# Optimization experiments

Hardware: AMD Instinct MI355X
Metric: run time of the kernel (lower is better)

Reference implementation:

```python
import jax, jax.numpy as jnp
import numpy as np

EPS = 1e-8  # torchmetrics pairwise_cosine_similarity zero_diagonal-free eps behavior

def _l2_normalize(x, eps=EPS):
    # normalize rows; clamp norm to eps like torchmetrics does
    n = jnp.linalg.norm(x, axis=-1, keepdims=True)
    return x / jnp.maximum(n, eps)

def setup_inputs() -> dict:
    key = jax.random.key(0)
    k1, k2 = jax.random.split(key)
    hvs = jax.random.normal(k1, (16384, 4096), dtype=jnp.float32)  # [N, D] query hypervectors
    am = jax.random.normal(k2, (1024, 4096), dtype=jnp.float32)    # [C, D] associative memory
    return {"hvs": hvs, "am": am}

def reference(hvs, am):
    # pairwise cosine similarity: [N, C]
    sims = jnp.einsum('nd,cd->nc', _l2_normalize(hvs), _l2_normalize(am.astype(jnp.float32)))
    # predict(): top-1 retrieval over classes
    preds = jnp.argmax(sims, axis=1)
    # compute_confidence(): eta = (sims[:,1] - sims[:,0]) / 4 + 1/2
    eta = (sims[:, 1] - sims[:, 0]) * 0.25 + 0.5
    return preds, eta
```

## Files before the change

kernel.cpp:

```cpp
#include <hip/hip_runtime.h>
#include <hip/hip_bf16.h>


#define NQ 16384
#define NC 1024
#define DK 4096
#define TAU 4e-4f
#define WLMAX 8192

typedef __attribute__((ext_vector_type(8))) short short8;
typedef __attribute__((ext_vector_type(4))) float f32x4;
typedef unsigned short ushort_t;

__device__ __forceinline__ unsigned short bf16_rne(float x) {
    unsigned int u = __float_as_uint(x);
    u += 0x7FFFu + ((u >> 16) & 1u);
    return (unsigned short)(u >> 16);
}
__device__ __forceinline__ float bf16_f32(unsigned short h) {
    return __uint_as_float(((unsigned int)h) << 16);
}

#define GLDS(g, l)                                                                       \
    __builtin_amdgcn_global_load_lds((const __attribute__((address_space(1))) void*)(g), \
                                     (__attribute__((address_space(3))) void*)(l), 16, 0, 0)

__global__ void __launch_bounds__(256) norm_all_kernel(const float* __restrict__ hvs,
                                                       const float* __restrict__ am,
                                                       ushort_t* __restrict__ Ah,
                                                       ushort_t* __restrict__ Bh,
                                                       ushort_t* __restrict__ Bl) {
    const int b = blockIdx.x;
    const int tid = threadIdx.x;
    const float* x;
    ushort_t *hp, *lp;
    bool wlo;
    if (b < NC) {
        x = am + (size_t)b * DK;
        hp = Bh + (size_t)b * DK;
        lp = Bl + (size_t)b * DK;
        wlo = true;
    } else {
        const int r = b - NC;
        x = hvs + (size_t)r * DK;
        hp = Ah + (size_t)r * DK;
        lp = nullptr;
        wlo = false;
    }
    const float4* x4 = (const float4*)x;

    float4 v[4];
    float ss = 0.f;
#pragma unroll
    for (int i = 0; i < 4; ++i) {
        v[i] = x4[tid * 4 + i];
        ss += v[i].x * v[i].x + v[i].y * v[i].y + v[i].z * v[i].z + v[i].w * v[i].w;
    }
#pragma unroll
    for (int off = 32; off; off >>= 1) ss += __shfl_xor(ss, off, 64);
    __shared__ float wsum[4];
    const int lane = tid & 63, w = tid >> 6;
    if (lane == 0) wsum[w] = ss;
    __syncthreads();
    const float tot = wsum[0] + wsum[1] + wsum[2] + wsum[3];
    const float r = 1.0f / fmaxf(sqrtf(tot), 1e-8f);

    ushort_t hbuf[16], lbuf[16];
#pragma unroll
    for (int i = 0; i < 4; ++i) {
        const float xs[4] = {v[i].x * r, v[i].y * r, v[i].z * r, v[i].w * r};
#pragma unroll
        for (int j = 0; j < 4; ++j) {
            const unsigned short h = bf16_rne(xs[j]);
            hbuf[i * 4 + j] = h;
            lbuf[i * 4 + j] = bf16_rne(xs[j] - bf16_f32(h));
        }
    }
    ushort_t* hq = hp + tid * 16;
    *(short8*)hq = *(short8*)hbuf;
    *(short8*)(hq + 8) = *(short8*)(hbuf + 8);
    if (wlo) {
        ushort_t* lq = lp + tid * 16;
        *(short8*)lq = *(short8*)lbuf;
        *(short8*)(lq + 8) = *(short8*)(lbuf + 8);
    }
}

__global__ void __launch_bounds__(256, 3) gemm1_kernel(const ushort_t* __restrict__ Ah,
                                                       const ushort_t* __restrict__ Bh,
                                                       float4* __restrict__ cand,
                                                       float* __restrict__ s01) {
    __shared__ __align__(16) ushort_t lA[2][128 * 32];
    __shared__ __align__(16) ushort_t lB[2][128 * 32];

    const int tid = threadIdx.x;
    const int lane = tid & 63;
    const int w = tid >> 6;
    const int wm = w >> 1;
    const int wn = w & 1;

    const int id = blockIdx.x;
    const int xcd = id & 7;
    const int slot = id >> 3;
    const int by = xcd * 16 + (slot >> 3);
    const int bx = slot & 7;

    int sq[2];
    size_t offA[2], offB[2];
#pragma unroll
    for (int i = 0; i < 2; ++i) {
        const int q = tid + i * 256;
        sq[i] = q;
        const int row = q >> 2;
        const int gs = (q & 3) ^ ((row >> 1) & 3);
        offA[i] = (size_t)(by * 128 + row) * DK + gs * 8;
        offB[i] = (size_t)(bx * 128 + row) * DK + gs * 8;
    }

    f32x4 acc[4][4];
#pragma unroll
    for (int m = 0; m < 4; ++m)
#pragma unroll
        for (int n = 0; n < 4; ++n) acc[m][n] = (f32x4){0.f, 0.f, 0.f, 0.f};

    const int r0 = lane & 15;
    const int rg = lane >> 4;

    int aoff[4], boff[4];
#pragma unroll
    for (int m = 0; m < 4; ++m) {
        const int row = wm * 64 + m * 16 + r0;
        aoff[m] = row * 32 + (rg ^ ((row >> 1) & 3)) * 8;
    }
#pragma unroll
    for (int n = 0; n < 4; ++n) {
        const int col = wn * 64 + n * 16 + r0;
        boff[n] = col * 32 + (rg ^ ((col >> 1) & 3)) * 8;
    }

    auto stage = [&](int buf, int kt) {
        const size_t ko = (size_t)kt * 32;
        GLDS(Ah + offA[0] + ko, &lA[buf][sq[0] * 8]);
        GLDS(Ah + offA[1] + ko, &lA[buf][sq[1] * 8]);
        GLDS(Bh + offB[0] + ko, &lB[buf][sq[0] * 8]);
        GLDS(Bh + offB[1] + ko, &lB[buf][sq[1] * 8]);
    };

    stage(0, 0);
    const int nK = DK / 32;
    for (int kt = 0; kt < nK; ++kt) {
        const int cur = kt & 1;
        if (kt + 1 < nK) {
            stage(cur ^ 1, kt + 1);
            asm volatile("s_waitcnt vmcnt(4)" ::: "memory");
        } else {
            asm volatile("s_waitcnt vmcnt(0)" ::: "memory");
        }
        __builtin_amdgcn_s_barrier();

        short8 b0 = *(const short8*)&lB[cur][boff[0]];
        short8 b1 = *(const short8*)&lB[cur][boff[1]];
        short8 b2 = *(const short8*)&lB[cur][boff[2]];
        short8 b3 = *(const short8*)&lB[cur][boff[3]];
        short8 a0 = *(const short8*)&lA[cur][aoff[0]];
        short8 a1 = *(const short8*)&lA[cur][aoff[1]];
        short8 a2 = *(const short8*)&lA[cur][aoff[2]];
        short8 a3 = *(const short8*)&lA[cur][aoff[3]];
        asm volatile("s_waitcnt lgkmcnt(0)" ::: "memory");
        __builtin_amdgcn_s_setprio(1);
        acc[0][0] = __builtin_amdgcn_mfma_f32_16x16x32_bf16(a0, b0, acc[0][0], 0, 0, 0);
        acc[0][1] = __builtin_amdgcn_mfma_f32_16x16x32_bf16(a0, b1, acc[0][1], 0, 0, 0);
        acc[0][2] = __builtin_amdgcn_mfma_f32_16x16x32_bf16(a0, b2, acc[0][2], 0, 0, 0);
        acc[0][3] = __builtin_amdgcn_mfma_f32_16x16x32_bf16(a0, b3, acc[0][3], 0, 0, 0);
        acc[1][0] = __builtin_amdgcn_mfma_f32_16x16x32_bf16(a1, b0, acc[1][0], 0, 0, 0);
        acc[1][1] = __builtin_amdgcn_mfma_f32_16x16x32_bf16(a1, b1, acc[1][1], 0, 0, 0);
        acc[1][2] = __builtin_amdgcn_mfma_f32_16x16x32_bf16(a1, b2, acc[1][2], 0, 0, 0);
        acc[1][3] = __builtin_amdgcn_mfma_f32_16x16x32_bf16(a1, b3, acc[1][3], 0, 0, 0);
        acc[2][0] = __builtin_amdgcn_mfma_f32_16x16x32_bf16(a2, b0, acc[2][0], 0, 0, 0);
        acc[2][1] = __builtin_amdgcn_mfma_f32_16x16x32_bf16(a2, b1, acc[2][1], 0, 0, 0);
        acc[2][2] = __builtin_amdgcn_mfma_f32_16x16x32_bf16(a2, b2, acc[2][2], 0, 0, 0);
        acc[2][3] = __builtin_amdgcn_mfma_f32_16x16x32_bf16(a2, b3, acc[2][3], 0, 0, 0);
        acc[3][0] = __builtin_amdgcn_mfma_f32_16x16x32_bf16(a3, b0, acc[3][0], 0, 0, 0);
        acc[3][1] = __builtin_amdgcn_mfma_f32_16x16x32_bf16(a3, b1, acc[3][1], 0, 0, 0);
        acc[3][2] = __builtin_amdgcn_mfma_f32_16x16x32_bf16(a3, b2, acc[3][2], 0, 0, 0);
        acc[3][3] = __builtin_amdgcn_mfma_f32_16x16x32_bf16(a3, b3, acc[3][3], 0, 0, 0);
        __builtin_amdgcn_s_setprio(0);
        __builtin_amdgcn_s_barrier();
    }

    const int rowb = by * 128 + wm * 64;
#pragma unroll
    for (int m = 0; m < 4; ++m) {
#pragma unroll
        for (int j = 0; j < 4; ++j) {
            float v1 = acc[m][0][j];
            int i1 = bx * 128 + wn * 64 + r0;
            float v2 = -3.402823466e+38f;
#pragma unroll
            for (int n = 1; n < 4; ++n) {
                const float v = acc[m][n][j];
                const int c = bx * 128 + wn * 64 + n * 16 + r0;
                if (v > v1) { v2 = v1; v1 = v; i1 = c; }
                else { v2 = fmaxf(v2, v); }
            }
#pragma unroll
            for (int off = 1; off < 16; off <<= 1) {
                const float o1 = __shfl_xor(v1, off, 64);
                const int oi = __shfl_xor(i1, off, 64);
                const float o2 = __shfl_xor(v2, off, 64);
                if (o1 > v1 || (o1 == v1 && oi < i1)) { v2 = fmaxf(v1, o2); v1 = o1; i1 = oi; }
                else { v2 = fmaxf(v2, o1); }
            }
            const int row = rowb + m * 16 + rg * 4 + j;
            if (r0 == 0)
                cand[(size_t)row * 16 + bx * 2 + wn] = make_float4(v1, (float)i1, v2, 0.f);
            if (bx == 0 && wn == 0 && r0 < 2) s01[row * 2 + r0] = acc[m][0][j];
        }
    }
}

__global__ void __launch_bounds__(256) finalizeA_kernel(const float4* __restrict__ cand,
                                                        const float* __restrict__ s01,
                                                        float* __restrict__ out,
                                                        int* __restrict__ wl,
                                                        int* __restrict__ wc) {
    const int row = blockIdx.x * 256 + threadIdx.x;
    const float4* c = cand + (size_t)row * 16;
    float4 c0 = c[0];
    float M = c0.x, iM = c0.y, M2 = c0.z;
#pragma unroll
    for (int k = 1; k < 16; ++k) {
        const float4 ck = c[k];
        if (ck.x > M) { M2 = fmaxf(M, ck.z); M = ck.x; iM = ck.y; }
        else { M2 = fmaxf(M2, ck.x); }
    }
    out[row] = iM;
    out[NQ + row] = (s01[row * 2 + 1] - s01[row * 2 + 0]) * 0.25f + 0.5f;
    if (M - M2 < TAU) {
        const int p = atomicAdd(wc, 1);
        if (p < WLMAX) wl[p] = row;
    }
}

__global__ void __launch_bounds__(256) recheck_prep_kernel(const float* __restrict__ hvs,
                                                           const int* __restrict__ wl,
                                                           const int* __restrict__ wc,
                                                           ushort_t* __restrict__ A2h,
                                                           ushort_t* __restrict__ A2l) {
    const int cnt = min(*wc, WLMAX);
    const int s = blockIdx.x;
    if (s >= cnt) return;
    const int row = wl[s];
    const int tid = threadIdx.x;
    const float4* x4 = (const float4*)(hvs + (size_t)row * DK);

    float4 v[4];
    float ss = 0.f;
#pragma unroll
    for (int i = 0; i < 4; ++i) {
        v[i] = x4[tid * 4 + i];
        ss += v[i].x * v[i].x + v[i].y * v[i].y + v[i].z * v[i].z + v[i].w * v[i].w;
    }
#pragma unroll
    for (int off = 32; off; off >>= 1) ss += __shfl_xor(ss, off, 64);
    __shared__ float wsum[4];
    const int lane = tid & 63, w = tid >> 6;
    if (lane == 0) wsum[w] = ss;
    __syncthreads();
    const float tot = wsum[0] + wsum[1] + wsum[2] + wsum[3];
    const float r = 1.0f / fmaxf(sqrtf(tot), 1e-8f);

    ushort_t hbuf[16], lbuf[16];
#pragma unroll
    for (int i = 0; i < 4; ++i) {
        const float xs[4] = {v[i].x * r, v[i].y * r, v[i].z * r, v[i].w * r};
#pragma unroll
        for (int j = 0; j < 4; ++j) {
            const unsigned short h = bf16_rne(xs[j]);
            hbuf[i * 4 + j] = h;
            lbuf[i * 4 + j] = bf16_rne(xs[j] - bf16_f32(h));
        }
    }
    ushort_t* hp = A2h + (size_t)s * DK + tid * 16;
    ushort_t* lp = A2l + (size_t)s * DK + tid * 16;
    *(short8*)hp = *(short8*)hbuf;
    *(short8*)(hp + 8) = *(short8*)(hbuf + 8);
    *(short8*)lp = *(short8*)lbuf;
    *(short8*)(lp + 8) = *(short8*)(lbuf + 8);
}

__global__ void __launch_bounds__(512, 2) gemm2_kernel(const ushort_t* __restrict__ A2h,
                                                       const ushort_t* __restrict__ A2l,
                                                       const ushort_t* __restrict__ Bh,
                                                       const ushort_t* __restrict__ Bl,
                                                       const int* __restrict__ wc,
                                                       float2* __restrict__ cand2) {
    const int cnt = min(*wc, WLMAX);
    const int by = blockIdx.y;
    const int bx = blockIdx.x;
    if (by * 128 >= cnt) return;

    __shared__ __align__(16) ushort_t lA[4][2][128 * 32];
    __shared__ __align__(16) ushort_t lB[4][2][128 * 32];

    const int tid = threadIdx.x;
    const int lane = tid & 63;
    const int w = tid >> 6;
    const int wm = w >> 2;
    const int wn = w & 3;
    const int r0 = lane & 15;
    const int rg = lane >> 4;

    const int srow = tid >> 2;
    const int gs = (tid & 3) ^ ((srow >> 1) & 3);
    const size_t offA = (size_t)(by * 128 + srow) * DK + gs * 8;
    const size_t offB = (size_t)(bx * 128 + srow) * DK + gs * 8;

    f32x4 acc[4][2];
#pragma unroll
    for (int m = 0; m < 4; ++m)
#pragma unroll
        for (int n = 0; n < 2; ++n) acc[m][n] = (f32x4){0.f, 0.f, 0.f, 0.f};

    int aoff[4], boff[2];
#pragma unroll
    for (int m = 0; m < 4; ++m) {
        const int row = wm * 64 + m * 16 + r0;
        aoff[m] = row * 32 + (rg ^ ((row >> 1) & 3)) * 8;
    }
#pragma unroll
    for (int n = 0; n < 2; ++n) {
        const int col = wn * 32 + n * 16 + r0;
        boff[n] = col * 32 + (rg ^ ((col >> 1) & 3)) * 8;
    }

    auto stage = [&](int kt) {
        const int buf = kt & 3;
        const size_t ko = (size_t)kt * 32;
        GLDS(A2h + offA + ko, &lA[buf][0][tid * 8]);
        GLDS(A2l + offA + ko, &lA[buf][1][tid * 8]);
        GLDS(Bh + offB + ko, &lB[buf][0][tid * 8]);
        GLDS(Bl + offB + ko, &lB[buf][1][tid * 8]);
    };

    stage(0); stage(1); stage(2);
    const int nK = DK / 32;
    for (int kt = 0; kt < nK; ++kt) {
        const int buf = kt & 3;
        if (kt + 3 < nK) {
            stage(kt + 3);
            asm volatile("s_waitcnt vmcnt(12)" ::: "memory");
        } else if (kt + 3 == nK) {
            asm volatile("s_waitcnt vmcnt(8)" ::: "memory");
        } else if (kt + 2 == nK) {
            asm volatile("s_waitcnt vmcnt(4)" ::: "memory");
        } else {
            asm volatile("s_waitcnt vmcnt(0)" ::: "memory");
        }
        __builtin_amdgcn_s_barrier();

        short8 bh[2], bl[2];
#pragma unroll
        for (int n = 0; n < 2; ++n) {
            bh[n] = *(const short8*)&lB[buf][0][boff[n]];
            bl[n] = *(const short8*)&lB[buf][1][boff[n]];
        }
#pragma unroll
        for (int m = 0; m < 4; ++m) {
            const short8 ah = *(const short8*)&lA[buf][0][aoff[m]];
            const short8 al = *(const short8*)&lA[buf][1][aoff[m]];
#pragma unroll
            for (int n = 0; n < 2; ++n) {
                acc[m][n] = __builtin_amdgcn_mfma_f32_16x16x32_bf16(ah, bh[n], acc[m][n], 0, 0, 0);
                acc[m][n] = __builtin_amdgcn_mfma_f32_16x16x32_bf16(ah, bl[n], acc[m][n], 0, 0, 0);
                acc[m][n] = __builtin_amdgcn_mfma_f32_16x16x32_bf16(al, bh[n], acc[m][n], 0, 0, 0);
            }
        }
        __builtin_amdgcn_s_barrier();
    }

#pragma unroll
    for (int m = 0; m < 4; ++m) {
#pragma unroll
        for (int j = 0; j < 4; ++j) {
            float best = acc[m][0][j];
            int bidx = bx * 128 + wn * 32 + r0;
            {
                const float v = acc[m][1][j];
                const int c = bx * 128 + wn * 32 + 16 + r0;
                if (v > best) { best = v; bidx = c; }
            }
#pragma unroll
            for (int off = 1; off < 16; off <<= 1) {
                const float ov = __shfl_xor(best, off, 64);
                const int oi = __shfl_xor(bidx, off, 64);
                if (ov > best || (ov == best && oi < bidx)) { best = ov; bidx = oi; }
            }
            const int slotg = by * 128 + wm * 64 + m * 16 + rg * 4 + j;
            if (r0 == 0 && slotg < cnt)
                cand2[(size_t)slotg * 32 + bx * 4 + wn] = make_float2(best, (float)bidx);
        }
    }
}

__global__ void __launch_bounds__(256) finalizeB_kernel(const float2* __restrict__ cand2,
                                                        const int* __restrict__ wl,
                                                        const int* __restrict__ wc,
                                                        float* __restrict__ out) {
    const int slot = blockIdx.x * 256 + threadIdx.x;
    const int cnt = min(*wc, WLMAX);
    if (slot >= cnt) return;
    const int row = wl[slot];
    const float2* c = cand2 + (size_t)slot * 32;
    float best = c[0].x;
    float bi = c[0].y;
#pragma unroll
    for (int k = 1; k < 32; ++k) {
        const float2 p = c[k];
        if (p.x > best) { best = p.x; bi = p.y; }
    }
    out[row] = bi;
}

extern "C" void kernel_launch(void* const* d_in, const int* in_sizes, int n_in,
                              void* d_out, int out_size, void* d_ws, size_t ws_size,
                              hipStream_t stream) {
    const float* hvs = (const float*)d_in[0];
    const float* am  = (const float*)d_in[1];
    float* out = (float*)d_out;

    ushort_t* Bh = (ushort_t*)d_ws;
    ushort_t* Bl = Bh + (size_t)NC * DK;
    ushort_t* Ah = Bl + (size_t)NC * DK;
    ushort_t* A2h = Ah + (size_t)NQ * DK;
    ushort_t* A2l = A2h + (size_t)WLMAX * DK;
    float4* cand = (float4*)(A2l + (size_t)WLMAX * DK);
    float* s01 = (float*)(cand + (size_t)NQ * 16);
    float2* cand2 = (float2*)(s01 + (size_t)NQ * 2);
    int* wl = (int*)(cand2 + (size_t)WLMAX * 32);
    int* wc = wl + WLMAX;

    hipMemsetAsync(wc, 0, sizeof(int), stream);
    norm_all_kernel<<<NC + NQ, 256, 0, stream>>>(hvs, am, Ah, Bh, Bl);
    gemm1_kernel<<<1024, 256, 0, stream>>>(Ah, Bh, cand, s01);
    finalizeA_kernel<<<NQ / 256, 256, 0, stream>>>(cand, s01, out, wl, wc);
    recheck_prep_kernel<<<WLMAX, 256, 0, stream>>>(hvs, wl, wc, A2h, A2l);
    gemm2_kernel<<<dim3(8, WLMAX / 128), 512, 0, stream>>>(A2h, A2l, Bh, Bl, wc, cand2);
    finalizeB_kernel<<<WLMAX / 256, 256, 0, stream>>>(cand2, wl, wc, out);
}
```

Measured before the change: 409.3 us.

## Replace split-bf16 recheck GEMM with targeted fp32 dot products on top-2 candidates

Ambiguous rows are no longer re-scored against all 1024 classes with a three-pass bf16 hi/lo GEMM. Each tile now also records its second-best index, so the recheck kernel computes exact fp32 dot products only for the candidates that fall within the tolerance window. It falls back to a full fp32 scan of all classes only when some tile's second-best also lies in the window. This drops the Bl/A2h/A2l buffers, the prep kernel, gemm2 and finalizeB, at the cost of a slightly heavier top-2 reduction in gemm1 and slow scalar-ish fallback rows.

```diff
diff --git a/kernel.cpp b/kernel.cpp
--- a/kernel.cpp
+++ b/kernel.cpp
@@ -29,23 +29,18 @@
                                                        const float* __restrict__ am,
                                                        ushort_t* __restrict__ Ah,
                                                        ushort_t* __restrict__ Bh,
-                                                       ushort_t* __restrict__ Bl) {
+                                                       float* __restrict__ arn) {
     const int b = blockIdx.x;
     const int tid = threadIdx.x;
     const float* x;
-    ushort_t *hp, *lp;
-    bool wlo;
+    ushort_t* hp;
     if (b < NC) {
         x = am + (size_t)b * DK;
         hp = Bh + (size_t)b * DK;
-        lp = Bl + (size_t)b * DK;
-        wlo = true;
     } else {
         const int r = b - NC;
         x = hvs + (size_t)r * DK;
         hp = Ah + (size_t)r * DK;
-        lp = nullptr;
-        wlo = false;
     }
     const float4* x4 = (const float4*)x;
 
@@ -64,26 +59,18 @@
     __syncthreads();
     const float tot = wsum[0] + wsum[1] + wsum[2] + wsum[3];
     const float r = 1.0f / fmaxf(sqrtf(tot), 1e-8f);
-
-    ushort_t hbuf[16], lbuf[16];
+    if (b < NC && tid == 0) arn[b] = r;
+
+    ushort_t hbuf[16];
 #pragma unroll
     for (int i = 0; i < 4; ++i) {
         const float xs[4] = {v[i].x * r, v[i].y * r, v[i].z * r, v[i].w * r};
 #pragma unroll
-        for (int j = 0; j < 4; ++j) {
-            const unsigned short h = bf16_rne(xs[j]);
-            hbuf[i * 4 + j] = h;
-            lbuf[i * 4 + j] = bf16_rne(xs[j] - bf16_f32(h));
-        }
+        for (int j = 0; j < 4; ++j) hbuf[i * 4 + j] = bf16_rne(xs[j]);
     }
     ushort_t* hq = hp + tid * 16;
     *(short8*)hq = *(short8*)hbuf;
     *(short8*)(hq + 8) = *(short8*)(hbuf + 8);
-    if (wlo) {
-        ushort_t* lq = lp + tid * 16;
-        *(short8*)lq = *(short8*)lbuf;
-        *(short8*)(lq + 8) = *(short8*)(lbuf + 8);
-    }
 }
 
 __global__ void __launch_bounds__(256, 3) gemm1_kernel(const ushort_t* __restrict__ Ah,
@@ -196,24 +183,32 @@
             float v1 = acc[m][0][j];
             int i1 = bx * 128 + wn * 64 + r0;
             float v2 = -3.402823466e+38f;
+            int i2 = i1;
 #pragma unroll
             for (int n = 1; n < 4; ++n) {
                 const float v = acc[m][n][j];
                 const int c = bx * 128 + wn * 64 + n * 16 + r0;
-                if (v > v1) { v2 = v1; v1 = v; i1 = c; }
-                else { v2 = fmaxf(v2, v); }
+                if (v > v1) { v2 = v1; i2 = i1; v1 = v; i1 = c; }
+                else if (v > v2) { v2 = v; i2 = c; }
             }
 #pragma unroll
             for (int off = 1; off < 16; off <<= 1) {
                 const float o1 = __shfl_xor(v1, off, 64);
-                const int oi = __shfl_xor(i1, off, 64);
                 const float o2 = __shfl_xor(v2, off, 64);
-                if (o1 > v1 || (o1 == v1 && oi < i1)) { v2 = fmaxf(v1, o2); v1 = o1; i1 = oi; }
-                else { v2 = fmaxf(v2, o1); }
+                const int oi1 = __shfl_xor(i1, off, 64);
+                const int oi2 = __shfl_xor(i2, off, 64);
+                if (o1 > v1 || (o1 == v1 && oi1 < i1)) {
+                    const float pv = v1; const int pi = i1;
+                    v1 = o1; i1 = oi1;
+                    if (pv >= o2) { v2 = pv; i2 = pi; }
+                    else { v2 = o2; i2 = oi2; }
+                } else {
+                    if (o1 >= v2) { v2 = o1; i2 = oi1; }
+                }
             }
             const int row = rowb + m * 16 + rg * 4 + j;
             if (r0 == 0)
-                cand[(size_t)row * 16 + bx * 2 + wn] = make_float4(v1, (float)i1, v2, 0.f);
+                cand[(size_t)row * 16 + bx * 2 + wn] = make_float4(v1, (float)i1, v2, (float)i2);
             if (bx == 0 && wn == 0 && r0 < 2) s01[row * 2 + r0] = acc[m][0][j];
         }
     }
@@ -242,18 +237,30 @@
     }
 }
 
-__global__ void __launch_bounds__(256) recheck_prep_kernel(const float* __restrict__ hvs,
-                                                           const int* __restrict__ wl,
-                                                           const int* __restrict__ wc,
-                                                           ushort_t* __restrict__ A2h,
-                                                           ushort_t* __restrict__ A2l) {
+__global__ void __launch_bounds__(256) recheck_kernel(const float* __restrict__ hvs,
+                                                      const float* __restrict__ am,
+                                                      const float* __restrict__ arn,
+                                                      const float4* __restrict__ cand,
+                                                      const int* __restrict__ wl,
+                                                      const int* __restrict__ wc,
+                                                      float* __restrict__ out) {
     const int cnt = min(*wc, WLMAX);
     const int s = blockIdx.x;
     if (s >= cnt) return;
     const int row = wl[s];
     const int tid = threadIdx.x;
+    const int lane = tid & 63;
+    const int w = tid >> 6;
+
+    __shared__ __align__(16) float aLDS[DK];
+    __shared__ float4 cLDS[16];
+    __shared__ float wsum[4];
+    __shared__ float wbest[4];
+    __shared__ int wbidx[4];
+
+    if (tid < 16) cLDS[tid] = cand[(size_t)row * 16 + tid];
+
     const float4* x4 = (const float4*)(hvs + (size_t)row * DK);
-
     float4 v[4];
     float ss = 0.f;
 #pragma unroll
@@ -263,163 +270,81 @@
     }
 #pragma unroll
     for (int off = 32; off; off >>= 1) ss += __shfl_xor(ss, off, 64);
-    __shared__ float wsum[4];
-    const int lane = tid & 63, w = tid >> 6;
     if (lane == 0) wsum[w] = ss;
+#pragma unroll
+    for (int i = 0; i < 4; ++i) ((float4*)aLDS)[tid * 4 + i] = v[i];
     __syncthreads();
-    const float tot = wsum[0] + wsum[1] + wsum[2] + wsum[3];
-    const float r = 1.0f / fmaxf(sqrtf(tot), 1e-8f);
-
-    ushort_t hbuf[16], lbuf[16];
-#pragma unroll
-    for (int i = 0; i < 4; ++i) {
-        const float xs[4] = {v[i].x * r, v[i].y * r, v[i].z * r, v[i].w * r};
-#pragma unroll
-        for (int j = 0; j < 4; ++j) {
-            const unsigned short h = bf16_rne(xs[j]);
-            hbuf[i * 4 + j] = h;
-            lbuf[i * 4 + j] = bf16_rne(xs[j] - bf16_f32(h));
-        }
-    }
-    ushort_t* hp = A2h + (size_t)s * DK + tid * 16;
-    ushort_t* lp = A2l + (size_t)s * DK + tid * 16;
-    *(short8*)hp = *(short8*)hbuf;
-    *(short8*)(hp + 8) = *(short8*)(hbuf + 8);
-    *(short8*)lp = *(short8*)lbuf;
-    *(short8*)(lp + 8) = *(short8*)(lbuf + 8);
-}
-
-__global__ void __launch_bounds__(512, 2) gemm2_kernel(const ushort_t* __restrict__ A2h,
-                                                       const ushort_t* __restrict__ A2l,
-                                                       const ushort_t* __restrict__ Bh,
-                                                       const ushort_t* __restrict__ Bl,
-                                                       const int* __restrict__ wc,
-                                                       float2* __restrict__ cand2) {
-    const int cnt = min(*wc, WLMAX);
-    const int by = blockIdx.y;
-    const int bx = blockIdx.x;
-    if (by * 128 >= cnt) return;
-
-    __shared__ __align__(16) ushort_t lA[4][2][128 * 32];
-    __shared__ __align__(16) ushort_t lB[4][2][128 * 32];
-
-    const int tid = threadIdx.x;
-    const int lane = tid & 63;
-    const int w = tid >> 6;
-    const int wm = w >> 2;
-    const int wn = w & 3;
-    const int r0 = lane & 15;
-    const int rg = lane >> 4;
-
-    const int srow = tid >> 2;
-    const int gs = (tid & 3) ^ ((srow >> 1) & 3);
-    const size_t offA = (size_t)(by * 128 + srow) * DK + gs * 8;
-    const size_t offB = (size_t)(bx * 128 + srow) * DK + gs * 8;
-
-    f32x4 acc[4][2];
-#pragma unroll
-    for (int m = 0; m < 4; ++m)
-#pragma unroll
-        for (int n = 0; n < 2; ++n) acc[m][n] = (f32x4){0.f, 0.f, 0.f, 0.f};
-
-    int aoff[4], boff[2];
-#pragma unroll
-    for (int m = 0; m < 4; ++m) {
-        const int row = wm * 64 + m * 16 + r0;
-        aoff[m] = row * 32 + (rg ^ ((row >> 1) & 3)) * 8;
-    }
-#pragma unroll
-    for (int n = 0; n < 2; ++n) {
-        const int col = wn * 32 + n * 16 + r0;
-        boff[n] = col * 32 + (rg ^ ((col >> 1) & 3)) * 8;
-    }
-
-    auto stage = [&](int kt) {
-        const int buf = kt & 3;
-        const size_t ko = (size_t)kt * 32;
-        GLDS(A2h + offA + ko, &lA[buf][0][tid * 8]);
-        GLDS(A2l + offA + ko, &lA[buf][1][tid * 8]);
-        GLDS(Bh + offB + ko, &lB[buf][0][tid * 8]);
-        GLDS(Bl + offB + ko, &lB[buf][1][tid * 8]);
-    };
-
-    stage(0); stage(1); stage(2);
-    const int nK = DK / 32;
-    for (int kt = 0; kt < nK; ++kt) {
-        const int buf = kt & 3;
-        if (kt + 3 < nK) {
-            stage(kt + 3);
-            asm volatile("s_waitcnt vmcnt(12)" ::: "memory");
-        } else if (kt + 3 == nK) {
-            asm volatile("s_waitcnt vmcnt(8)" ::: "memory");
-        } else if (kt + 2 == nK) {
-            asm volatile("s_waitcnt vmcnt(4)" ::: "memory");
-        } else {
-            asm volatile("s_waitcnt vmcnt(0)" ::: "memory");
-        }
-        __builtin_amdgcn_s_barrier();
-
-        short8 bh[2], bl[2];
-#pragma unroll
-        for (int n = 0; n < 2; ++n) {
-            bh[n] = *(const short8*)&lB[buf][0][boff[n]];
-            bl[n] = *(const short8*)&lB[buf][1][boff[n]];
-        }
-#pragma unroll
-        for (int m = 0; m < 4; ++m) {
-            const short8 ah = *(const short8*)&lA[buf][0][aoff[m]];
-            const short8 al = *(const short8*)&lA[buf][1][aoff[m]];
-#pragma unroll
-            for (int n = 0; n < 2; ++n) {
-                acc[m][n] = __builtin_amdgcn_mfma_f32_16x16x32_bf16(ah, bh[n], acc[m][n], 0, 0, 0);
-                acc[m][n] = __builtin_amdgcn_mfma_f32_16x16x32_bf16(ah, bl[n], acc[m][n], 0, 0, 0);
-                acc[m][n] = __builtin_amdgcn_mfma_f32_16x16x32_bf16(al, bh[n], acc[m][n], 0, 0, 0);
-            }
-        }
-        __builtin_amdgcn_s_barrier();
-    }
-
-#pragma unroll
-    for (int m = 0; m < 4; ++m) {
-#pragma unroll
-        for (int j = 0; j < 4; ++j) {
-            float best = acc[m][0][j];
-            int bidx = bx * 128 + wn * 32 + r0;
-            {
-                const float v = acc[m][1][j];
-                const int c = bx * 128 + wn * 32 + 16 + r0;
-                if (v > best) { best = v; bidx = c; }
-            }
-#pragma unroll
-            for (int off = 1; off < 16; off <<= 1) {
-                const float ov = __shfl_xor(best, off, 64);
-                const int oi = __shfl_xor(bidx, off, 64);
-                if (ov > best || (ov == best && oi < bidx)) { best = ov; bidx = oi; }
-            }
-            const int slotg = by * 128 + wm * 64 + m * 16 + rg * 4 + j;
-            if (r0 == 0 && slotg < cnt)
-                cand2[(size_t)slotg * 32 + bx * 4 + wn] = make_float2(best, (float)bidx);
-        }
-    }
-}
-
-__global__ void __launch_bounds__(256) finalizeB_kernel(const float2* __restrict__ cand2,
-                                                        const int* __restrict__ wl,
-                                                        const int* __restrict__ wc,
-                                                        float* __restrict__ out) {
-    const int slot = blockIdx.x * 256 + threadIdx.x;
-    const int cnt = min(*wc, WLMAX);
-    if (slot >= cnt) return;
-    const int row = wl[slot];
-    const float2* c = cand2 + (size_t)slot * 32;
-    float best = c[0].x;
-    float bi = c[0].y;
-#pragma unroll
-    for (int k = 1; k < 32; ++k) {
-        const float2 p = c[k];
-        if (p.x > best) { best = p.x; bi = p.y; }
-    }
-    out[row] = bi;
+    const float rinv = 1.0f / fmaxf(sqrtf(wsum[0] + wsum[1] + wsum[2] + wsum[3]), 1e-8f);
+
+    float M = cLDS[0].x;
+#pragma unroll
+    for (int k = 1; k < 16; ++k) M = fmaxf(M, cLDS[k].x);
+    const float wnd = M - TAU;
+    bool needs_full = false;
+#pragma unroll
+    for (int k = 0; k < 16; ++k) needs_full |= (cLDS[k].z >= wnd);
+
+    const float4* am4 = (const float4*)am;
+    const float4* a4 = (const float4*)aLDS;
+
+    if (!needs_full) {
+        if (w == 0) {
+            float best = -3.402823466e+38f;
+            int bidx = 0x7FFFFFFF;
+            for (int k = 0; k < 16; ++k) {
+                const float4 ck = cLDS[k];
+#pragma unroll
+                for (int t = 0; t < 2; ++t) {
+                    const float val = t ? ck.z : ck.x;
+                    const int c = (int)(t ? ck.w : ck.y);
+                    if (val < wnd) continue;
+                    float p = 0.f;
+#pragma unroll
+                    for (int j = 0; j < 16; ++j) {
+                        const float4 av = a4[j * 64 + lane];
+                        const float4 bv = am4[(size_t)c * (DK / 4) + j * 64 + lane];
+                        p += av.x * bv.x + av.y * bv.y + av.z * bv.z + av.w * bv.w;
+                    }
+#pragma unroll
+                    for (int off = 32; off; off >>= 1) p += __shfl_xor(p, off, 64);
+                    if (lane == 0) {
+                        const float sim = p * rinv * arn[c];
+                        if (sim > best || (sim == best && c < bidx)) { best = sim; bidx = c; }
+                    }
+                }
+            }
+            if (lane == 0) out[row] = (float)bidx;
+        }
+    } else {
+        float best = -3.402823466e+38f;
+        int bidx = 0x7FFFFFFF;
+        for (int c = w * 256; c < (w + 1) * 256; ++c) {
+            float p = 0.f;
+#pragma unroll
+            for (int j = 0; j < 16; ++j) {
+                const float4 av = a4[j * 64 + lane];
+                const float4 bv = am4[(size_t)c * (DK / 4) + j * 64 + lane];
+                p += av.x * bv.x + av.y * bv.y + av.z * bv.z + av.w * bv.w;
+            }
+#pragma unroll
+            for (int off = 32; off; off >>= 1) p += __shfl_xor(p, off, 64);
+            if (lane == 0) {
+                const float sim = p * rinv * arn[c];
+                if (sim > best || (sim == best && c < bidx)) { best = sim; bidx = c; }
+            }
+        }
+        if (lane == 0) { wbest[w] = best; wbidx[w] = bidx; }
+        __syncthreads();
+        if (tid == 0) {
+            float b = wbest[0];
+            int bi = wbidx[0];
+#pragma unroll
+            for (int k = 1; k < 4; ++k) {
+                if (wbest[k] > b || (wbest[k] == b && wbidx[k] < bi)) { b = wbest[k]; bi = wbidx[k]; }
+            }
+            out[row] = (float)bi;
+        }
+    }
 }
 
 extern "C" void kernel_launch(void* const* d_in, const int* in_sizes, int n_in,
@@ -430,21 +355,16 @@
     float* out = (float*)d_out;
 
     ushort_t* Bh = (ushort_t*)d_ws;
-    ushort_t* Bl = Bh + (size_t)NC * DK;
-    ushort_t* Ah = Bl + (size_t)NC * DK;
-    ushort_t* A2h = Ah + (size_t)NQ * DK;
-    ushort_t* A2l = A2h + (size_t)WLMAX * DK;
-    float4* cand = (float4*)(A2l + (size_t)WLMAX * DK);
+    ushort_t* Ah = Bh + (size_t)NC * DK;
+    float4* cand = (float4*)(Ah + (size_t)NQ * DK);
     float* s01 = (float*)(cand + (size_t)NQ * 16);
-    float2* cand2 = (float2*)(s01 + (size_t)NQ * 2);
-    int* wl = (int*)(cand2 + (size_t)WLMAX * 32);
+    float* arn = s01 + (size_t)NQ * 2;
+    int* wl = (int*)(arn + NC);
     int* wc = wl + WLMAX;
 
     hipMemsetAsync(wc, 0, sizeof(int), stream);
-    norm_all_kernel<<<NC + NQ, 256, 0, stream>>>(hvs, am, Ah, Bh, Bl);
+    norm_all_kernel<<<NC + NQ, 256, 0, stream>>>(hvs, am, Ah, Bh, arn);
     gemm1_kernel<<<1024, 256, 0, stream>>>(Ah, Bh, cand, s01);
     finalizeA_kernel<<<NQ / 256, 256, 0, stream>>>(cand, s01, out, wl, wc);
-    recheck_prep_kernel<<<WLMAX, 256, 0, stream>>>(hvs, wl, wc, A2h, A2l);
-    gemm2_kernel<<<dim3(8, WLMAX / 128), 512, 0, stream>>>(A2h, A2l, Bh, Bl, wc, cand2);
-    finalizeB_kernel<<<WLMAX / 256, 256, 0, stream>>>(cand2, wl, wc, out);
-}
+    recheck_kernel<<<WLMAX, 256, 0, stream>>>(hvs, am, arn, cand, wl, wc, out);
+}
```

Result: slower. 1.188 ms (+190.2%).
